# Optimization experiments

Hardware: AMD Instinct MI355X
Metric: run time of the kernel (lower is better)

The kernel has to match this reference:

```python
import jax, jax.numpy as jnp
import numpy as np

N = 1024
D = 128            # hidden_dim
TEMPERATURE = 1.0
SPARSE_K = 32


def setup_inputs() -> dict:
    key = jax.random.key(0)
    ks = jax.random.split(key, 10)
    s = 1.0 / np.sqrt(D)
    s2 = 1.0 / np.sqrt(2 * D)
    z = jax.random.normal(ks[0], (N, D), dtype=jnp.float32)
    spatial_dist = jax.random.uniform(ks[1], (N, N), dtype=jnp.float32)
    # Linear weights stored as [in, out] (transposed vs torch) so y = x @ W + b
    Wq = jax.random.normal(ks[2], (D, D), dtype=jnp.float32) * s
    bq = jnp.zeros((D,), dtype=jnp.float32)
    Wk = jax.random.normal(ks[3], (D, D), dtype=jnp.float32) * s
    bk = jnp.zeros((D,), dtype=jnp.float32)
    W1 = jax.random.normal(ks[4], (2 * D, D), dtype=jnp.float32) * s2
    b1 = jnp.zeros((D,), dtype=jnp.float32)
    W2 = jax.random.normal(ks[5], (D, 3), dtype=jnp.float32) * s
    b2 = jnp.zeros((3,), dtype=jnp.float32)
    return {"z": z, "spatial_dist": spatial_dist, "Wq": Wq, "bq": bq,
            "Wk": Wk, "bk": bk, "W1": W1, "b1": b1, "W2": W2, "b2": b2}


def reference(z, spatial_dist, Wq, bq, Wk, bk, W1, b1, W2, b2):
    n = z.shape[0]
    # ---- attention adjacency ----
    Q = z @ Wq + bq                                   # [N, D]
    K = z @ Wk + bk                                   # [N, D]
    attn = (Q @ K.T) * (1.0 / (D ** 0.5)) / TEMPERATURE   # [N, N]
    attn = attn * jnp.exp(-spatial_dist)              # spatial weighting
    adjacency = jax.nn.softmax(attn, axis=-1)
    # top-k sparsification (scatter top-k values into zeros)
    topk_vals, topk_idx = jax.lax.top_k(adjacency, SPARSE_K)   # [N, k]
    rows = jnp.arange(n)[:, None]
    adjacency = jnp.zeros_like(adjacency).at[rows, topk_idx].set(topk_vals)
    # ---- pairwise signaling-type classifier ----
    a = z @ W1[:D]                                    # [N, D]
    b = z @ W1[D:]                                    # [N, D]
    h = jax.nn.gelu(a[:, None, :] + b[None, :, :] + b1, approximate=False)  # [N, N, D]
    logits = jnp.einsum('ijd,dc->ijc', h, W2) + b2    # [N, N, 3]
    signaling_type = jax.nn.softmax(logits, axis=-1)
    return adjacency, signaling_type
```

## Files before the change

kernel.cpp:

```cpp
#include <hip/hip_runtime.h>
#include <hip/hip_fp16.h>

#define N 1024
#define D 128

__global__ __launch_bounds__(256) void proj_kernel(
    const float* __restrict__ z,
    const float* __restrict__ Wq, const float* __restrict__ bq,
    const float* __restrict__ Wk, const float* __restrict__ bk,
    const float* __restrict__ W1, const float* __restrict__ b1,
    __half* __restrict__ Qh, __half* __restrict__ Kh,
    __half* __restrict__ Ah, __half* __restrict__ Bh)
{
    const int d  = threadIdx.x & (D - 1);
    const int h  = threadIdx.x >> 7;
    const int r0 = blockIdx.x * 4;
    const float* __restrict__ Wa = h ? W1           : Wq;
    const float* __restrict__ Wb = h ? (W1 + D * D) : Wk;

    float acc0[4] = {0,0,0,0};
    float acc1[4] = {0,0,0,0};

    for (int c = 0; c < D / 4; ++c) {
        float4 zr[4];
#pragma unroll
        for (int r = 0; r < 4; ++r)
            zr[r] = *(const float4*)&z[(r0 + r) * D + c * 4];
#pragma unroll
        for (int q = 0; q < 4; ++q) {
            const int k = c * 4 + q;
            const float wa = Wa[k * D + d];
            const float wb = Wb[k * D + d];
#pragma unroll
            for (int r = 0; r < 4; ++r) {
                const float zv = (q == 0) ? zr[r].x : (q == 1) ? zr[r].y : (q == 2) ? zr[r].z : zr[r].w;
                acc0[r] = fmaf(zv, wa, acc0[r]);
                acc1[r] = fmaf(zv, wb, acc1[r]);
            }
        }
    }
    if (h == 0) {
        const float c0 = bq[d], c1 = bk[d];
        const float scale = 0.08838834764831845f;
#pragma unroll
        for (int r = 0; r < 4; ++r) {
            Qh[(r0 + r) * D + d] = __float2half((acc0[r] + c0) * scale);
            Kh[(r0 + r) * D + d] = __float2half(acc1[r] + c1);
        }
    } else {
        const float c0 = b1[d];
#pragma unroll
        for (int r = 0; r < 4; ++r) {
            Ah[(r0 + r) * D + d] = __float2half(acc0[r] + c0);
            Bh[(r0 + r) * D + d] = __float2half(acc1[r]);
        }
    }
}

union H2x4 { uint4 u; __half2 h[4]; };

__device__ __forceinline__ float fdot2_acc(__half2 a, __half2 b, float c) {
#if __has_builtin(__builtin_amdgcn_fdot2)
    typedef _Float16 v2h __attribute__((ext_vector_type(2)));
    union { __half2 h; v2h v; } ua, ub;
    ua.h = a; ub.h = b;
    return __builtin_amdgcn_fdot2(ua.v, ub.v, c, false);
#else
    return fmaf(__low2float(a), __low2float(b),
           fmaf(__high2float(a), __high2float(b), c));
#endif
}

#define HP 136

__global__ __launch_bounds__(256) void score_kernel(
    const __half* __restrict__ Qh, const __half* __restrict__ Kh,
    const float* __restrict__ dist, float* __restrict__ S)
{
    __shared__ __align__(16) __half Qs[32 * HP];
    __shared__ __align__(16) __half Ks[32 * HP];
    const int tid = threadIdx.x;
    const int bi = blockIdx.y * 32, bj = blockIdx.x * 32;
    const int tx = tid & 15, ty = tid >> 4;

#pragma unroll
    for (int t = 0; t < 2; ++t) {
        const int e = t * 256 + tid;
        const int row = e >> 4, c = e & 15;
        *(uint4*)&Qs[row * HP + c * 8] = *(const uint4*)&Qh[(size_t)(bi + row) * D + c * 8];
        *(uint4*)&Ks[row * HP + c * 8] = *(const uint4*)&Kh[(size_t)(bj + row) * D + c * 8];
    }
    __syncthreads();

    float a00 = 0.f, a01 = 0.f, a10 = 0.f, a11 = 0.f;

#pragma unroll 4
    for (int c = 0; c < 16; ++c) {
        H2x4 q0, q1, k0, k1;
        q0.u = *(const uint4*)&Qs[ty * HP + c * 8];
        q1.u = *(const uint4*)&Qs[(ty + 16) * HP + c * 8];
        k0.u = *(const uint4*)&Ks[tx * HP + c * 8];
        k1.u = *(const uint4*)&Ks[(tx + 16) * HP + c * 8];
#pragma unroll
        for (int dp = 0; dp < 4; ++dp) {
            a00 = fdot2_acc(q0.h[dp], k0.h[dp], a00);
            a01 = fdot2_acc(q0.h[dp], k1.h[dp], a01);
            a10 = fdot2_acc(q1.h[dp], k0.h[dp], a10);
            a11 = fdot2_acc(q1.h[dp], k1.h[dp], a11);
        }
    }

    const int i0 = bi + ty, i1 = bi + ty + 16;
    const int j0 = bj + tx, j1 = bj + tx + 16;
    S[(size_t)i0 * N + j0] = a00 * __expf(-dist[(size_t)i0 * N + j0]);
    S[(size_t)i0 * N + j1] = a01 * __expf(-dist[(size_t)i0 * N + j1]);
    S[(size_t)i1 * N + j0] = a10 * __expf(-dist[(size_t)i1 * N + j0]);
    S[(size_t)i1 * N + j1] = a11 * __expf(-dist[(size_t)i1 * N + j1]);
}

__global__ __launch_bounds__(256) void topk_kernel(float* buf)
{
    const int lane = threadIdx.x & 63;
    const int row  = blockIdx.x * 4 + (threadIdx.x >> 6);
    float* sr = buf + (size_t)row * N;

    float v[16];
#pragma unroll
    for (int c = 0; c < 4; ++c) {
        const float4 f = *(const float4*)&sr[(c * 64 + lane) * 4];
        v[c * 4 + 0] = f.x; v[c * 4 + 1] = f.y; v[c * 4 + 2] = f.z; v[c * 4 + 3] = f.w;
    }
    float m = v[0];
#pragma unroll
    for (int e = 1; e < 16; ++e) m = fmaxf(m, v[e]);
#pragma unroll
    for (int off = 1; off < 64; off <<= 1) m = fmaxf(m, __shfl_xor(m, off));
    float sum = 0.f;
#pragma unroll
    for (int e = 0; e < 16; ++e) sum += __expf(v[e] - m);
#pragma unroll
    for (int off = 1; off < 64; off <<= 1) sum += __shfl_xor(sum, off);
    const float inv = 1.0f / sum;

    unsigned key[16];
#pragma unroll
    for (int e = 0; e < 16; ++e) {
        const int j = (((e >> 2) * 64 + lane) * 4) + (e & 3);
        unsigned u = __float_as_uint(v[e]);
        u = (u & 0x80000000u) ? ~u : (u | 0x80000000u);
        key[e] = (u & 0xFFFFFC00u) | (unsigned)(N - 1 - j);
    }
    unsigned flags = 0;
    for (int it = 0; it < 32; ++it) {
        unsigned best = key[0];
#pragma unroll
        for (int e = 1; e < 16; ++e) best = (key[e] > best) ? key[e] : best;
#pragma unroll
        for (int off = 1; off < 64; off <<= 1) {
            const unsigned o = __shfl_xor(best, off);
            if (o > best) best = o;
        }
#pragma unroll
        for (int e = 0; e < 16; ++e)
            if (key[e] == best) { flags |= 1u << e; key[e] = 0u; }
    }
#pragma unroll
    for (int c = 0; c < 4; ++c) {
        float4 o;
        o.x = (flags & (1u << (c * 4 + 0))) ? __expf(v[c * 4 + 0] - m) * inv : 0.f;
        o.y = (flags & (1u << (c * 4 + 1))) ? __expf(v[c * 4 + 1] - m) * inv : 0.f;
        o.z = (flags & (1u << (c * 4 + 2))) ? __expf(v[c * 4 + 2] - m) * inv : 0.f;
        o.w = (flags & (1u << (c * 4 + 3))) ? __expf(v[c * 4 + 3] - m) * inv : 0.f;
        *(float4*)&sr[(c * 64 + lane) * 4] = o;
    }
}

__global__ __launch_bounds__(256) void pair_kernel(
    const __half* __restrict__ Ah, const __half* __restrict__ Bh,
    const float* __restrict__ W2, const float* __restrict__ b2,
    float* __restrict__ out)
{
    __shared__ __align__(16) __half AsH[32 * HP];
    __shared__ __align__(16) __half BsH[32 * HP];
    __shared__ __align__(16) __half2 Wh[2][68];
    const int tid = threadIdx.x;
    const int bi = blockIdx.y * 32, bj = blockIdx.x * 32;
    const int tx = tid & 15, ty = tid >> 4;

#pragma unroll
    for (int t = 0; t < 2; ++t) {
        const int e = t * 256 + tid;
        const int row = e >> 4, c = e & 15;
        *(uint4*)&AsH[row * HP + c * 8] = *(const uint4*)&Ah[(size_t)(bi + row) * D + c * 8];
        *(uint4*)&BsH[row * HP + c * 8] = *(const uint4*)&Bh[(size_t)(bj + row) * D + c * 8];
    }
    if (tid < 128) {
        const int cls = tid >> 6, dp = tid & 63;
        Wh[cls][dp] = __floats2half2_rn(W2[6 * dp + cls]     - W2[6 * dp + 2],
                                        W2[6 * dp + 3 + cls] - W2[6 * dp + 5]);
    }
    const float bb0 = b2[0] - b2[2], bb1 = b2[1] - b2[2];
    __syncthreads();

    float acc[4][2];
#pragma unroll
    for (int p = 0; p < 4; ++p) { acc[p][0] = bb0; acc[p][1] = bb1; }

    const __half2 C3  = __float2half2_rn(-0.1029434f);
    const __half2 C1  = __float2half2_rn(-2.3022082f);
    const __half2 ONE = __float2half2_rn(1.0f);

#pragma unroll 4
    for (int c = 0; c < 16; ++c) {
        H2x4 a0, a1, b0, b1, w0, w1;
        a0.u = *(const uint4*)&AsH[ty * HP + c * 8];
        a1.u = *(const uint4*)&AsH[(ty + 16) * HP + c * 8];
        b0.u = *(const uint4*)&BsH[tx * HP + c * 8];
        b1.u = *(const uint4*)&BsH[(tx + 16) * HP + c * 8];
        w0.u = *(const uint4*)&Wh[0][c * 4];
        w1.u = *(const uint4*)&Wh[1][c * 4];
#pragma unroll
        for (int dp = 0; dp < 4; ++dp) {
            const __half2 aa[2] = { a0.h[dp], a1.h[dp] };
            const __half2 bb[2] = { b0.h[dp], b1.h[dp] };
            const __half2 wc0 = w0.h[dp], wc1 = w1.h[dp];
#pragma unroll
            for (int ii = 0; ii < 2; ++ii)
#pragma unroll
                for (int jj = 0; jj < 2; ++jj) {
                    const __half2 x = __hadd2(aa[ii], bb[jj]);
                    const __half2 u = __hmul2(x, x);
                    const __half2 p = __hfma2(C3, u, C1);
                    const __half2 t = __hmul2(x, p);
                    const __half2 e = h2exp2(t);
                    const __half2 dn = __hadd2(e, ONE);
                    const __half2 r = h2rcp(dn);
                    const __half2 g = __hmul2(x, r);
                    float* l = acc[ii * 2 + jj];
                    l[0] = fdot2_acc(g, wc0, l[0]);
                    l[1] = fdot2_acc(g, wc1, l[1]);
                }
        }
    }

#pragma unroll
    for (int ii = 0; ii < 2; ++ii)
#pragma unroll
        for (int jj = 0; jj < 2; ++jj) {
            const int i = bi + ty + 16 * ii;
            const int j = bj + tx + 16 * jj;
            const float* l = acc[ii * 2 + jj];
            const float l0 = l[0], l1 = l[1];
            const float mm = fmaxf(fmaxf(l0, l1), 0.f);
            const float e0 = __expf(l0 - mm), e1 = __expf(l1 - mm), e2 = __expf(-mm);
            const float inv2 = 1.0f / (e0 + e1 + e2);
            float* o = out + ((size_t)i * N + j) * 3;
            o[0] = e0 * inv2; o[1] = e1 * inv2; o[2] = e2 * inv2;
        }
}

extern "C" void kernel_launch(void* const* d_in, const int* in_sizes, int n_in,
                              void* d_out, int out_size, void* d_ws, size_t ws_size,
                              hipStream_t stream)
{
    const float* z    = (const float*)d_in[0];
    const float* dist = (const float*)d_in[1];
    const float* Wq   = (const float*)d_in[2];
    const float* bq   = (const float*)d_in[3];
    const float* Wk   = (const float*)d_in[4];
    const float* bk   = (const float*)d_in[5];
    const float* W1   = (const float*)d_in[6];
    const float* b1   = (const float*)d_in[7];
    const float* W2   = (const float*)d_in[8];
    const float* b2   = (const float*)d_in[9];

    float* out = (float*)d_out;
    __half* Qh = (__half*)d_ws;
    __half* Kh = Qh + (size_t)N * D;
    __half* Ah = Kh + (size_t)N * D;
    __half* Bh = Ah + (size_t)N * D;

    proj_kernel<<<N / 4, 256, 0, stream>>>(z, Wq, bq, Wk, bk, W1, b1, Qh, Kh, Ah, Bh);
    score_kernel<<<dim3(N / 32, N / 32), 256, 0, stream>>>(Qh, Kh, dist, out);
    topk_kernel<<<N / 4, 256, 0, stream>>>(out);
    pair_kernel<<<dim3(N / 32, N / 32), 256, 0, stream>>>(Ah, Bh, W2, b2, out + (size_t)N * N);
}
```

Baseline: 142.9 us.

## Fuse attention score computation with softmax and top-k into one row kernel

Merges the score kernel and the top-k kernel into a single kernel where each wavefront owns one query row held in registers. K is streamed through XOR-swizzled shared memory in 64-row chunks with register prefetch, so the NxN score matrix no longer takes a global write and read-back round trip and one launch disappears. The cost is lower parallelism (256 blocks), since each block rereads all of K, and loop-carried synchronization per chunk. Output stores become scalar, but each store is still coalesced across lanes.

```diff
diff --git a/kernel.cpp b/kernel.cpp
--- a/kernel.cpp
+++ b/kernel.cpp
@@ -71,65 +71,61 @@
 #endif
 }
 
-#define HP 136
-
-__global__ __launch_bounds__(256) void score_kernel(
+__global__ __launch_bounds__(256) void score_topk_kernel(
     const __half* __restrict__ Qh, const __half* __restrict__ Kh,
-    const float* __restrict__ dist, float* __restrict__ S)
-{
-    __shared__ __align__(16) __half Qs[32 * HP];
-    __shared__ __align__(16) __half Ks[32 * HP];
-    const int tid = threadIdx.x;
-    const int bi = blockIdx.y * 32, bj = blockIdx.x * 32;
-    const int tx = tid & 15, ty = tid >> 4;
-
-#pragma unroll
-    for (int t = 0; t < 2; ++t) {
-        const int e = t * 256 + tid;
-        const int row = e >> 4, c = e & 15;
-        *(uint4*)&Qs[row * HP + c * 8] = *(const uint4*)&Qh[(size_t)(bi + row) * D + c * 8];
-        *(uint4*)&Ks[row * HP + c * 8] = *(const uint4*)&Kh[(size_t)(bj + row) * D + c * 8];
-    }
-    __syncthreads();
-
-    float a00 = 0.f, a01 = 0.f, a10 = 0.f, a11 = 0.f;
-
-#pragma unroll 4
+    const float* __restrict__ dist, float* __restrict__ out)
+{
+    __shared__ __align__(16) uint4 Ks[64 * 16];
+    const int tid  = threadIdx.x;
+    const int lane = tid & 63;
+    const int row  = blockIdx.x * 4 + (tid >> 6);
+
+    uint4 qreg[16];
+#pragma unroll
+    for (int k = 0; k < 16; ++k)
+        qreg[k] = *(const uint4*)&Qh[(size_t)row * D + k * 8];
+
+    uint4 pre[4];
+#pragma unroll
+    for (int t = 0; t < 4; ++t) {
+        const int e = t * 256 + tid, r = e >> 4, col = e & 15;
+        pre[t] = *(const uint4*)&Kh[(size_t)r * D + col * 8];
+    }
+
+    float v[16];
     for (int c = 0; c < 16; ++c) {
-        H2x4 q0, q1, k0, k1;
-        q0.u = *(const uint4*)&Qs[ty * HP + c * 8];
-        q1.u = *(const uint4*)&Qs[(ty + 16) * HP + c * 8];
-        k0.u = *(const uint4*)&Ks[tx * HP + c * 8];
-        k1.u = *(const uint4*)&Ks[(tx + 16) * HP + c * 8];
-#pragma unroll
-        for (int dp = 0; dp < 4; ++dp) {
-            a00 = fdot2_acc(q0.h[dp], k0.h[dp], a00);
-            a01 = fdot2_acc(q0.h[dp], k1.h[dp], a01);
-            a10 = fdot2_acc(q1.h[dp], k0.h[dp], a10);
-            a11 = fdot2_acc(q1.h[dp], k1.h[dp], a11);
-        }
-    }
-
-    const int i0 = bi + ty, i1 = bi + ty + 16;
-    const int j0 = bj + tx, j1 = bj + tx + 16;
-    S[(size_t)i0 * N + j0] = a00 * __expf(-dist[(size_t)i0 * N + j0]);
-    S[(size_t)i0 * N + j1] = a01 * __expf(-dist[(size_t)i0 * N + j1]);
-    S[(size_t)i1 * N + j0] = a10 * __expf(-dist[(size_t)i1 * N + j0]);
-    S[(size_t)i1 * N + j1] = a11 * __expf(-dist[(size_t)i1 * N + j1]);
-}
-
-__global__ __launch_bounds__(256) void topk_kernel(float* buf)
-{
-    const int lane = threadIdx.x & 63;
-    const int row  = blockIdx.x * 4 + (threadIdx.x >> 6);
-    float* sr = buf + (size_t)row * N;
-
-    float v[16];
-#pragma unroll
-    for (int c = 0; c < 4; ++c) {
-        const float4 f = *(const float4*)&sr[(c * 64 + lane) * 4];
-        v[c * 4 + 0] = f.x; v[c * 4 + 1] = f.y; v[c * 4 + 2] = f.z; v[c * 4 + 3] = f.w;
-    }
+        __syncthreads();
+#pragma unroll
+        for (int t = 0; t < 4; ++t) {
+            const int e = t * 256 + tid, r = e >> 4, col = e & 15;
+            Ks[r * 16 + (col ^ (r & 15))] = pre[t];
+        }
+        __syncthreads();
+        if (c < 15) {
+#pragma unroll
+            for (int t = 0; t < 4; ++t) {
+                const int e = t * 256 + tid, r = e >> 4, col = e & 15;
+                pre[t] = *(const uint4*)&Kh[(size_t)((c + 1) * 64 + r) * D + col * 8];
+            }
+        }
+        float s[4] = {0.f, 0.f, 0.f, 0.f};
+#pragma unroll
+        for (int k = 0; k < 4; ++k)
+#pragma unroll
+            for (int mm = 0; mm < 4; ++mm) {
+                const int c8 = k * 4 + mm;
+                H2x4 kk, qq;
+                kk.u = Ks[lane * 16 + (c8 ^ (lane & 15))];
+                qq.u = qreg[c8];
+                s[k] = fdot2_acc(qq.h[0], kk.h[0], s[k]);
+                s[k] = fdot2_acc(qq.h[1], kk.h[1], s[k]);
+                s[k] = fdot2_acc(qq.h[2], kk.h[2], s[k]);
+                s[k] = fdot2_acc(qq.h[3], kk.h[3], s[k]);
+            }
+        const int j = c * 64 + lane;
+        v[c] = ((s[0] + s[1]) + (s[2] + s[3])) * __expf(-dist[(size_t)row * N + j]);
+    }
+
     float m = v[0];
 #pragma unroll
     for (int e = 1; e < 16; ++e) m = fmaxf(m, v[e]);
@@ -145,7 +141,7 @@
     unsigned key[16];
 #pragma unroll
     for (int e = 0; e < 16; ++e) {
-        const int j = (((e >> 2) * 64 + lane) * 4) + (e & 3);
+        const int j = e * 64 + lane;
         unsigned u = __float_as_uint(v[e]);
         u = (u & 0x80000000u) ? ~u : (u | 0x80000000u);
         key[e] = (u & 0xFFFFFC00u) | (unsigned)(N - 1 - j);
@@ -165,15 +161,13 @@
             if (key[e] == best) { flags |= 1u << e; key[e] = 0u; }
     }
 #pragma unroll
-    for (int c = 0; c < 4; ++c) {
-        float4 o;
-        o.x = (flags & (1u << (c * 4 + 0))) ? __expf(v[c * 4 + 0] - m) * inv : 0.f;
-        o.y = (flags & (1u << (c * 4 + 1))) ? __expf(v[c * 4 + 1] - m) * inv : 0.f;
-        o.z = (flags & (1u << (c * 4 + 2))) ? __expf(v[c * 4 + 2] - m) * inv : 0.f;
-        o.w = (flags & (1u << (c * 4 + 3))) ? __expf(v[c * 4 + 3] - m) * inv : 0.f;
-        *(float4*)&sr[(c * 64 + lane) * 4] = o;
-    }
-}
+    for (int e = 0; e < 16; ++e) {
+        const float o = (flags & (1u << e)) ? __expf(v[e] - m) * inv : 0.f;
+        out[(size_t)row * N + e * 64 + lane] = o;
+    }
+}
+
+#define HP 136
 
 __global__ __launch_bounds__(256) void pair_kernel(
     const __half* __restrict__ Ah, const __half* __restrict__ Bh,
@@ -281,7 +275,6 @@
     __half* Bh = Ah + (size_t)N * D;
 
     proj_kernel<<<N / 4, 256, 0, stream>>>(z, Wq, bq, Wk, bk, W1, b1, Qh, Kh, Ah, Bh);
-    score_kernel<<<dim3(N / 32, N / 32), 256, 0, stream>>>(Qh, Kh, dist, out);
-    topk_kernel<<<N / 4, 256, 0, stream>>>(out);
+    score_topk_kernel<<<N / 4, 256, 0, stream>>>(Qh, Kh, dist, out);
     pair_kernel<<<dim3(N / 32, N / 32), 256, 0, stream>>>(Ah, Bh, W2, b2, out + (size_t)N * N);
 }
```

After: 175.2 us. 22.5% more time.

## Fuse score, top-k and pair kernels into one launch with per-row-block counters

Applied to the files above, without the earlier changes.

Merges the score, top-k and pairwise classifier kernels into a single grid. The first half of the blocks compute score tiles, and the last block to finish each row band, tracked by an atomic counter, runs the softmax/top-k for those 32 rows. The second half of the blocks compute the pair classifier concurrently. This removes two kernel launches and lets the serial top-k tail overlap with the heavy pair work. In exchange it adds threadfence/atomic overhead and puts the top-k work on only 32 blocks running 8 rows per wave each, which could become a long tail. Counters are reset in the projection kernel.

```diff
diff --git a/kernel.cpp b/kernel.cpp
--- a/kernel.cpp
+++ b/kernel.cpp
@@ -10,8 +10,11 @@
     const float* __restrict__ Wk, const float* __restrict__ bk,
     const float* __restrict__ W1, const float* __restrict__ b1,
     __half* __restrict__ Qh, __half* __restrict__ Kh,
-    __half* __restrict__ Ah, __half* __restrict__ Bh)
+    __half* __restrict__ Ah, __half* __restrict__ Bh,
+    unsigned* __restrict__ cnt)
 {
+    if (blockIdx.x == 0 && threadIdx.x < 32) cnt[threadIdx.x] = 0;
+
     const int d  = threadIdx.x & (D - 1);
     const int h  = threadIdx.x >> 7;
     const int r0 = blockIdx.x * 4;
@@ -73,190 +76,197 @@
 
 #define HP 136
 
-__global__ __launch_bounds__(256) void score_kernel(
+__global__ __launch_bounds__(256) void fused_kernel(
     const __half* __restrict__ Qh, const __half* __restrict__ Kh,
-    const float* __restrict__ dist, float* __restrict__ S)
-{
-    __shared__ __align__(16) __half Qs[32 * HP];
-    __shared__ __align__(16) __half Ks[32 * HP];
-    const int tid = threadIdx.x;
-    const int bi = blockIdx.y * 32, bj = blockIdx.x * 32;
-    const int tx = tid & 15, ty = tid >> 4;
-
-#pragma unroll
-    for (int t = 0; t < 2; ++t) {
-        const int e = t * 256 + tid;
-        const int row = e >> 4, c = e & 15;
-        *(uint4*)&Qs[row * HP + c * 8] = *(const uint4*)&Qh[(size_t)(bi + row) * D + c * 8];
-        *(uint4*)&Ks[row * HP + c * 8] = *(const uint4*)&Kh[(size_t)(bj + row) * D + c * 8];
-    }
-    __syncthreads();
-
-    float a00 = 0.f, a01 = 0.f, a10 = 0.f, a11 = 0.f;
-
-#pragma unroll 4
-    for (int c = 0; c < 16; ++c) {
-        H2x4 q0, q1, k0, k1;
-        q0.u = *(const uint4*)&Qs[ty * HP + c * 8];
-        q1.u = *(const uint4*)&Qs[(ty + 16) * HP + c * 8];
-        k0.u = *(const uint4*)&Ks[tx * HP + c * 8];
-        k1.u = *(const uint4*)&Ks[(tx + 16) * HP + c * 8];
-#pragma unroll
-        for (int dp = 0; dp < 4; ++dp) {
-            a00 = fdot2_acc(q0.h[dp], k0.h[dp], a00);
-            a01 = fdot2_acc(q0.h[dp], k1.h[dp], a01);
-            a10 = fdot2_acc(q1.h[dp], k0.h[dp], a10);
-            a11 = fdot2_acc(q1.h[dp], k1.h[dp], a11);
-        }
-    }
-
-    const int i0 = bi + ty, i1 = bi + ty + 16;
-    const int j0 = bj + tx, j1 = bj + tx + 16;
-    S[(size_t)i0 * N + j0] = a00 * __expf(-dist[(size_t)i0 * N + j0]);
-    S[(size_t)i0 * N + j1] = a01 * __expf(-dist[(size_t)i0 * N + j1]);
-    S[(size_t)i1 * N + j0] = a10 * __expf(-dist[(size_t)i1 * N + j0]);
-    S[(size_t)i1 * N + j1] = a11 * __expf(-dist[(size_t)i1 * N + j1]);
-}
-
-__global__ __launch_bounds__(256) void topk_kernel(float* buf)
-{
-    const int lane = threadIdx.x & 63;
-    const int row  = blockIdx.x * 4 + (threadIdx.x >> 6);
-    float* sr = buf + (size_t)row * N;
-
-    float v[16];
-#pragma unroll
-    for (int c = 0; c < 4; ++c) {
-        const float4 f = *(const float4*)&sr[(c * 64 + lane) * 4];
-        v[c * 4 + 0] = f.x; v[c * 4 + 1] = f.y; v[c * 4 + 2] = f.z; v[c * 4 + 3] = f.w;
-    }
-    float m = v[0];
-#pragma unroll
-    for (int e = 1; e < 16; ++e) m = fmaxf(m, v[e]);
-#pragma unroll
-    for (int off = 1; off < 64; off <<= 1) m = fmaxf(m, __shfl_xor(m, off));
-    float sum = 0.f;
-#pragma unroll
-    for (int e = 0; e < 16; ++e) sum += __expf(v[e] - m);
-#pragma unroll
-    for (int off = 1; off < 64; off <<= 1) sum += __shfl_xor(sum, off);
-    const float inv = 1.0f / sum;
-
-    unsigned key[16];
-#pragma unroll
-    for (int e = 0; e < 16; ++e) {
-        const int j = (((e >> 2) * 64 + lane) * 4) + (e & 3);
-        unsigned u = __float_as_uint(v[e]);
-        u = (u & 0x80000000u) ? ~u : (u | 0x80000000u);
-        key[e] = (u & 0xFFFFFC00u) | (unsigned)(N - 1 - j);
-    }
-    unsigned flags = 0;
-    for (int it = 0; it < 32; ++it) {
-        unsigned best = key[0];
-#pragma unroll
-        for (int e = 1; e < 16; ++e) best = (key[e] > best) ? key[e] : best;
-#pragma unroll
-        for (int off = 1; off < 64; off <<= 1) {
-            const unsigned o = __shfl_xor(best, off);
-            if (o > best) best = o;
-        }
-#pragma unroll
-        for (int e = 0; e < 16; ++e)
-            if (key[e] == best) { flags |= 1u << e; key[e] = 0u; }
-    }
-#pragma unroll
-    for (int c = 0; c < 4; ++c) {
-        float4 o;
-        o.x = (flags & (1u << (c * 4 + 0))) ? __expf(v[c * 4 + 0] - m) * inv : 0.f;
-        o.y = (flags & (1u << (c * 4 + 1))) ? __expf(v[c * 4 + 1] - m) * inv : 0.f;
-        o.z = (flags & (1u << (c * 4 + 2))) ? __expf(v[c * 4 + 2] - m) * inv : 0.f;
-        o.w = (flags & (1u << (c * 4 + 3))) ? __expf(v[c * 4 + 3] - m) * inv : 0.f;
-        *(float4*)&sr[(c * 64 + lane) * 4] = o;
-    }
-}
-
-__global__ __launch_bounds__(256) void pair_kernel(
+    const float* __restrict__ dist,
     const __half* __restrict__ Ah, const __half* __restrict__ Bh,
     const float* __restrict__ W2, const float* __restrict__ b2,
-    float* __restrict__ out)
+    unsigned* __restrict__ cnt, float* __restrict__ out)
 {
-    __shared__ __align__(16) __half AsH[32 * HP];
-    __shared__ __align__(16) __half BsH[32 * HP];
-    __shared__ __align__(16) __half2 Wh[2][68];
+    __shared__ __align__(16) unsigned char lds[18496];
+    __shared__ unsigned s_old;
     const int tid = threadIdx.x;
-    const int bi = blockIdx.y * 32, bj = blockIdx.x * 32;
     const int tx = tid & 15, ty = tid >> 4;
 
-#pragma unroll
-    for (int t = 0; t < 2; ++t) {
-        const int e = t * 256 + tid;
-        const int row = e >> 4, c = e & 15;
-        *(uint4*)&AsH[row * HP + c * 8] = *(const uint4*)&Ah[(size_t)(bi + row) * D + c * 8];
-        *(uint4*)&BsH[row * HP + c * 8] = *(const uint4*)&Bh[(size_t)(bj + row) * D + c * 8];
+    if (blockIdx.y < 32) {
+        __half* Qs = (__half*)lds;
+        __half* Ks = (__half*)(lds + 8704);
+        const int bi = blockIdx.y * 32, bj = blockIdx.x * 32;
+
+#pragma unroll
+        for (int t = 0; t < 2; ++t) {
+            const int e = t * 256 + tid;
+            const int row = e >> 4, c = e & 15;
+            *(uint4*)&Qs[row * HP + c * 8] = *(const uint4*)&Qh[(size_t)(bi + row) * D + c * 8];
+            *(uint4*)&Ks[row * HP + c * 8] = *(const uint4*)&Kh[(size_t)(bj + row) * D + c * 8];
+        }
+        __syncthreads();
+
+        float a00 = 0.f, a01 = 0.f, a10 = 0.f, a11 = 0.f;
+#pragma unroll 4
+        for (int c = 0; c < 16; ++c) {
+            H2x4 q0, q1, k0, k1;
+            q0.u = *(const uint4*)&Qs[ty * HP + c * 8];
+            q1.u = *(const uint4*)&Qs[(ty + 16) * HP + c * 8];
+            k0.u = *(const uint4*)&Ks[tx * HP + c * 8];
+            k1.u = *(const uint4*)&Ks[(tx + 16) * HP + c * 8];
+#pragma unroll
+            for (int dp = 0; dp < 4; ++dp) {
+                a00 = fdot2_acc(q0.h[dp], k0.h[dp], a00);
+                a01 = fdot2_acc(q0.h[dp], k1.h[dp], a01);
+                a10 = fdot2_acc(q1.h[dp], k0.h[dp], a10);
+                a11 = fdot2_acc(q1.h[dp], k1.h[dp], a11);
+            }
+        }
+        const int i0 = bi + ty, i1 = bi + ty + 16;
+        const int j0 = bj + tx, j1 = bj + tx + 16;
+        out[(size_t)i0 * N + j0] = a00 * __expf(-dist[(size_t)i0 * N + j0]);
+        out[(size_t)i0 * N + j1] = a01 * __expf(-dist[(size_t)i0 * N + j1]);
+        out[(size_t)i1 * N + j0] = a10 * __expf(-dist[(size_t)i1 * N + j0]);
+        out[(size_t)i1 * N + j1] = a11 * __expf(-dist[(size_t)i1 * N + j1]);
+
+        __threadfence();
+        __syncthreads();
+        if (tid == 0) s_old = atomicAdd(&cnt[blockIdx.y], 1u);
+        __syncthreads();
+        if (s_old == 31u) {
+            __threadfence();
+            const int wv = tid >> 6, lane = tid & 63;
+            for (int r8 = 0; r8 < 8; ++r8) {
+                const int row = bi + wv * 8 + r8;
+                float* sr = out + (size_t)row * N;
+
+                float v[16];
+#pragma unroll
+                for (int c = 0; c < 4; ++c) {
+                    const float4 f = *(const float4*)&sr[(c * 64 + lane) * 4];
+                    v[c * 4 + 0] = f.x; v[c * 4 + 1] = f.y; v[c * 4 + 2] = f.z; v[c * 4 + 3] = f.w;
+                }
+                float m = v[0];
+#pragma unroll
+                for (int e = 1; e < 16; ++e) m = fmaxf(m, v[e]);
+#pragma unroll
+                for (int off = 1; off < 64; off <<= 1) m = fmaxf(m, __shfl_xor(m, off));
+                float sum = 0.f;
+#pragma unroll
+                for (int e = 0; e < 16; ++e) sum += __expf(v[e] - m);
+#pragma unroll
+                for (int off = 1; off < 64; off <<= 1) sum += __shfl_xor(sum, off);
+                const float inv = 1.0f / sum;
+
+                unsigned key[16];
+#pragma unroll
+                for (int e = 0; e < 16; ++e) {
+                    const int j = (((e >> 2) * 64 + lane) * 4) + (e & 3);
+                    unsigned u = __float_as_uint(v[e]);
+                    u = (u & 0x80000000u) ? ~u : (u | 0x80000000u);
+                    key[e] = (u & 0xFFFFFC00u) | (unsigned)(N - 1 - j);
+                }
+                unsigned flags = 0;
+                for (int it = 0; it < 32; ++it) {
+                    unsigned best = key[0];
+#pragma unroll
+                    for (int e = 1; e < 16; ++e) best = (key[e] > best) ? key[e] : best;
+#pragma unroll
+                    for (int off = 1; off < 64; off <<= 1) {
+                        const unsigned o = __shfl_xor(best, off);
+                        if (o > best) best = o;
+                    }
+#pragma unroll
+                    for (int e = 0; e < 16; ++e)
+                        if (key[e] == best) { flags |= 1u << e; key[e] = 0u; }
+                }
+#pragma unroll
+                for (int c = 0; c < 4; ++c) {
+                    float4 o;
+                    o.x = (flags & (1u << (c * 4 + 0))) ? __expf(v[c * 4 + 0] - m) * inv : 0.f;
+                    o.y = (flags & (1u << (c * 4 + 1))) ? __expf(v[c * 4 + 1] - m) * inv : 0.f;
+                    o.z = (flags & (1u << (c * 4 + 2))) ? __expf(v[c * 4 + 2] - m) * inv : 0.f;
+                    o.w = (flags & (1u << (c * 4 + 3))) ? __expf(v[c * 4 + 3] - m) * inv : 0.f;
+                    *(float4*)&sr[(c * 64 + lane) * 4] = o;
+                }
+            }
+        }
+    } else {
+        __half*  AsH = (__half*)lds;
+        __half*  BsH = (__half*)(lds + 8704);
+        __half2* Wh0 = (__half2*)(lds + 17408);
+        __half2* Wh1 = Wh0 + 68;
+        const int bi = (blockIdx.y - 32) * 32, bj = blockIdx.x * 32;
+        float* pout = out + (size_t)N * N;
+
+#pragma unroll
+        for (int t = 0; t < 2; ++t) {
+            const int e = t * 256 + tid;
+            const int row = e >> 4, c = e & 15;
+            *(uint4*)&AsH[row * HP + c * 8] = *(const uint4*)&Ah[(size_t)(bi + row) * D + c * 8];
+            *(uint4*)&BsH[row * HP + c * 8] = *(const uint4*)&Bh[(size_t)(bj + row) * D + c * 8];
+        }
+        if (tid < 128) {
+            const int cls = tid >> 6, dp = tid & 63;
+            __half2* Wh = cls ? Wh1 : Wh0;
+            Wh[dp] = __floats2half2_rn(W2[6 * dp + cls]     - W2[6 * dp + 2],
+                                       W2[6 * dp + 3 + cls] - W2[6 * dp + 5]);
+        }
+        const float bb0 = b2[0] - b2[2], bb1 = b2[1] - b2[2];
+        __syncthreads();
+
+        float acc[4][2];
+#pragma unroll
+        for (int p = 0; p < 4; ++p) { acc[p][0] = bb0; acc[p][1] = bb1; }
+
+        const __half2 C3  = __float2half2_rn(-0.1029434f);
+        const __half2 C1  = __float2half2_rn(-2.3022082f);
+        const __half2 ONE = __float2half2_rn(1.0f);
+
+#pragma unroll 4
+        for (int c = 0; c < 16; ++c) {
+            H2x4 a0, a1, b0, b1, w0, w1;
+            a0.u = *(const uint4*)&AsH[ty * HP + c * 8];
+            a1.u = *(const uint4*)&AsH[(ty + 16) * HP + c * 8];
+            b0.u = *(const uint4*)&BsH[tx * HP + c * 8];
+            b1.u = *(const uint4*)&BsH[(tx + 16) * HP + c * 8];
+            w0.u = *(const uint4*)&Wh0[c * 4];
+            w1.u = *(const uint4*)&Wh1[c * 4];
+#pragma unroll
+            for (int dp = 0; dp < 4; ++dp) {
+                const __half2 aa[2] = { a0.h[dp], a1.h[dp] };
+                const __half2 bb[2] = { b0.h[dp], b1.h[dp] };
+                const __half2 wc0 = w0.h[dp], wc1 = w1.h[dp];
+#pragma unroll
+                for (int ii = 0; ii < 2; ++ii)
+#pragma unroll
+                    for (int jj = 0; jj < 2; ++jj) {
+                        const __half2 x = __hadd2(aa[ii], bb[jj]);
+                        const __half2 u = __hmul2(x, x);
+                        const __half2 p = __hfma2(C3, u, C1);
+                        const __half2 t = __hmul2(x, p);
+                        const __half2 e = h2exp2(t);
+                        const __half2 dn = __hadd2(e, ONE);
+                        const __half2 r = h2rcp(dn);
+                        const __half2 g = __hmul2(x, r);
+                        float* l = acc[ii * 2 + jj];
+                        l[0] = fdot2_acc(g, wc0, l[0]);
+                        l[1] = fdot2_acc(g, wc1, l[1]);
+                    }
+            }
+        }
+
+#pragma unroll
+        for (int ii = 0; ii < 2; ++ii)
+#pragma unroll
+            for (int jj = 0; jj < 2; ++jj) {
+                const int i = bi + ty + 16 * ii;
+                const int j = bj + tx + 16 * jj;
+                const float* l = acc[ii * 2 + jj];
+                const float l0 = l[0], l1 = l[1];
+                const float mm = fmaxf(fmaxf(l0, l1), 0.f);
+                const float e0 = __expf(l0 - mm), e1 = __expf(l1 - mm), e2 = __expf(-mm);
+                const float inv2 = 1.0f / (e0 + e1 + e2);
+                float* o = pout + ((size_t)i * N + j) * 3;
+                o[0] = e0 * inv2; o[1] = e1 * inv2; o[2] = e2 * inv2;
+            }
     }
-    if (tid < 128) {
-        const int cls = tid >> 6, dp = tid & 63;
-        Wh[cls][dp] = __floats2half2_rn(W2[6 * dp + cls]     - W2[6 * dp + 2],
-                                        W2[6 * dp + 3 + cls] - W2[6 * dp + 5]);
-    }
-    const float bb0 = b2[0] - b2[2], bb1 = b2[1] - b2[2];
-    __syncthreads();
-
-    float acc[4][2];
-#pragma unroll
-    for (int p = 0; p < 4; ++p) { acc[p][0] = bb0; acc[p][1] = bb1; }
-
-    const __half2 C3  = __float2half2_rn(-0.1029434f);
-    const __half2 C1  = __float2half2_rn(-2.3022082f);
-    const __half2 ONE = __float2half2_rn(1.0f);
-
-#pragma unroll 4
-    for (int c = 0; c < 16; ++c) {
-        H2x4 a0, a1, b0, b1, w0, w1;
-        a0.u = *(const uint4*)&AsH[ty * HP + c * 8];
-        a1.u = *(const uint4*)&AsH[(ty + 16) * HP + c * 8];
-        b0.u = *(const uint4*)&BsH[tx * HP + c * 8];
-        b1.u = *(const uint4*)&BsH[(tx + 16) * HP + c * 8];
-        w0.u = *(const uint4*)&Wh[0][c * 4];
-        w1.u = *(const uint4*)&Wh[1][c * 4];
-#pragma unroll
-        for (int dp = 0; dp < 4; ++dp) {
-            const __half2 aa[2] = { a0.h[dp], a1.h[dp] };
-            const __half2 bb[2] = { b0.h[dp], b1.h[dp] };
-            const __half2 wc0 = w0.h[dp], wc1 = w1.h[dp];
-#pragma unroll
-            for (int ii = 0; ii < 2; ++ii)
-#pragma unroll
-                for (int jj = 0; jj < 2; ++jj) {
-                    const __half2 x = __hadd2(aa[ii], bb[jj]);
-                    const __half2 u = __hmul2(x, x);
-                    const __half2 p = __hfma2(C3, u, C1);
-                    const __half2 t = __hmul2(x, p);
-                    const __half2 e = h2exp2(t);
-                    const __half2 dn = __hadd2(e, ONE);
-                    const __half2 r = h2rcp(dn);
-                    const __half2 g = __hmul2(x, r);
-                    float* l = acc[ii * 2 + jj];
-                    l[0] = fdot2_acc(g, wc0, l[0]);
-                    l[1] = fdot2_acc(g, wc1, l[1]);
-                }
-        }
-    }
-
-#pragma unroll
-    for (int ii = 0; ii < 2; ++ii)
-#pragma unroll
-        for (int jj = 0; jj < 2; ++jj) {
-            const int i = bi + ty + 16 * ii;
-            const int j = bj + tx + 16 * jj;
-            const float* l = acc[ii * 2 + jj];
-            const float l0 = l[0], l1 = l[1];
-            const float mm = fmaxf(fmaxf(l0, l1), 0.f);
-            const float e0 = __expf(l0 - mm), e1 = __expf(l1 - mm), e2 = __expf(-mm);
-            const float inv2 = 1.0f / (e0 + e1 + e2);
-            float* o = out + ((size_t)i * N + j) * 3;
-            o[0] = e0 * inv2; o[1] = e1 * inv2; o[2] = e2 * inv2;
-        }
 }
 
 extern "C" void kernel_launch(void* const* d_in, const int* in_sizes, int n_in,
@@ -279,9 +289,8 @@
     __half* Kh = Qh + (size_t)N * D;
     __half* Ah = Kh + (size_t)N * D;
     __half* Bh = Ah + (size_t)N * D;
-
-    proj_kernel<<<N / 4, 256, 0, stream>>>(z, Wq, bq, Wk, bk, W1, b1, Qh, Kh, Ah, Bh);
-    score_kernel<<<dim3(N / 32, N / 32), 256, 0, stream>>>(Qh, Kh, dist, out);
-    topk_kernel<<<N / 4, 256, 0, stream>>>(out);
-    pair_kernel<<<dim3(N / 32, N / 32), 256, 0, stream>>>(Ah, Bh, W2, b2, out + (size_t)N * N);
-}
+    unsigned* cnt = (unsigned*)(Bh + (size_t)N * D);
+
+    proj_kernel<<<N / 4, 256, 0, stream>>>(z, Wq, bq, Wk, bk, W1, b1, Qh, Kh, Ah, Bh, cnt);
+    fused_kernel<<<dim3(32, 64), 256, 0, stream>>>(Qh, Kh, dist, Ah, Bh, W2, b2, cnt, out);
+}
```

Result: slower. 351.2 us (+145.7%).
